# Kernel optimization log

Measured on AMD Instinct MI355X. Metric: run time of the kernel, lower is better.

Reference implementation:

```python
import jax, jax.numpy as jnp
import numpy as np

EPS = 1e-20


def setup_inputs() -> dict:
    B, N, V = 64, 8, 128000
    key = jax.random.key(0)
    k1, k2, k3 = jax.random.split(key, 3)
    draft_token_ids = jax.random.randint(k1, (B, N), 0, V, dtype=jnp.int64 if jax.config.jax_enable_x64 else jnp.int32)
    # proper probability distributions via softmax over random logits
    draft_probs = jax.nn.softmax(jax.random.normal(k2, (B, N, V), dtype=jnp.float32), axis=-1)
    verify_probs = jax.nn.softmax(jax.random.normal(k3, (B, N + 1, V), dtype=jnp.float32), axis=-1)
    return {
        "draft_token_ids": draft_token_ids,
        "draft_probs": draft_probs,
        "verify_probs": verify_probs,
    }


def reference(draft_token_ids, draft_probs, verify_probs):
    """Chain speculative (rejection) sampling, flashinfer-style.

    Returns:
      output_token_ids:  (B, N+1) int, rejected tail padded with -1
      accepted_token_num:(B,) independent per-token acceptance count
      emitted_token_num: (B,) accepted draft tokens before first rejection
    """
    B, N, V = draft_probs.shape
    key = jax.random.key(1)
    ku, kr, kb = jax.random.split(key, 3)

    tgt = verify_probs[:, :N, :]  # target probs aligned with draft positions
    # gather p = target prob of drafted token, q = draft prob of drafted token
    tok = draft_token_ids[..., None]
    p = jnp.take_along_axis(tgt, tok, axis=2)[..., 0]          # (B, N)
    q = jnp.take_along_axis(draft_probs, tok, axis=2)[..., 0]  # (B, N)

    u = jax.random.uniform(ku, (B, N), dtype=jnp.float32)
    accept = u * q < p                                          # (B, N) bool

    # independent-acceptance metric (alignment of draft vs target)
    accepted_token_num = accept.sum(axis=1).astype(jnp.int32)
    # chain: stop at first rejection
    prefix = jnp.cumprod(accept.astype(jnp.int32), axis=1)      # (B, N)
    emitted_token_num = prefix.sum(axis=1).astype(jnp.int32)    # (B,)

    # recovered distribution at each position: normalize relu(target - draft)
    residual = jnp.maximum(tgt - draft_probs, 0.0)
    residual = residual / jnp.maximum(residual.sum(axis=-1, keepdims=True), EPS)
    recovered = jax.random.categorical(kr, jnp.log(residual + EPS), axis=-1)  # (B, N)

    # bonus token from the extra target distribution (all drafts accepted)
    bonus = jax.random.categorical(kb, jnp.log(verify_probs[:, N, :] + EPS), axis=-1)  # (B,)

    batch_idx = jnp.arange(B)
    rec_at_stop = recovered[batch_idx, jnp.minimum(emitted_token_num, N - 1)]
    final_tok = jnp.where(emitted_token_num < N, rec_at_stop, bonus)  # (B,)

    pos = jnp.arange(N + 1)[None, :]                      # (1, N+1)
    em = emitted_token_num[:, None]                       # (B, 1)
    draft_ext = jnp.concatenate([draft_token_ids, jnp.zeros((B, 1), draft_token_ids.dtype)], axis=1)
    out = jnp.where(pos < em, draft_ext,
                    jnp.where(pos == em, final_tok[:, None].astype(draft_ext.dtype), -1))
    return out, accepted_token_num, emitted_token_num
```

## Files before the change

### kernel.cpp

```cpp
#include <hip/hip_runtime.h>
#include <stdint.h>

constexpr int Bn = 64;
constexpr int Nn = 8;
constexpr int Vn = 128000;
constexpr int CH = 32;
constexpr int CHUNK = Vn / CH;
constexpr int F4 = CHUNK / 4;
constexpr float EPSf = 1e-20f;
constexpr float TINYf = 1.17549435082228751e-38f;

struct TFOut { uint32_t a, b; };

__host__ __device__ constexpr TFOut tf2x32(uint32_t k0, uint32_t k1,
                                           uint32_t x0, uint32_t x1) {
  uint32_t k2 = k0 ^ k1 ^ 0x1BD11BDAu;
  x0 += k0; x1 += k1;
#define TFR(r) { x0 += x1; x1 = (uint32_t)((x1 << (r)) | (x1 >> (32 - (r)))); x1 ^= x0; }
  TFR(13) TFR(15) TFR(26) TFR(6)
  x0 += k1; x1 += k2 + 1u;
  TFR(17) TFR(29) TFR(16) TFR(24)
  x0 += k2; x1 += k0 + 2u;
  TFR(13) TFR(15) TFR(26) TFR(6)
  x0 += k0; x1 += k1 + 3u;
  TFR(17) TFR(29) TFR(16) TFR(24)
  x0 += k1; x1 += k2 + 4u;
  TFR(13) TFR(15) TFR(26) TFR(6)
  x0 += k2; x1 += k0 + 5u;
#undef TFR
  return TFOut{x0, x1};
}

constexpr TFOut KU = tf2x32(0u, 1u, 0u, 0u);
constexpr TFOut KR = tf2x32(0u, 1u, 0u, 1u);
constexpr TFOut KB_ = tf2x32(0u, 1u, 0u, 2u);

__device__ __forceinline__ float jax_u01(uint32_t bits) {
  return __uint_as_float((bits >> 9) | 0x3f800000u) - 1.0f;
}

__device__ __forceinline__ uint32_t rbits(uint32_t k0, uint32_t k1, uint32_t t) {
  TFOut o = tf2x32(k0, k1, 0u, t);
  return o.a ^ o.b;
}

__device__ __forceinline__ float gumbel_at(uint32_t k0, uint32_t k1, uint32_t t) {
  float u = jax_u01(rbits(k0, k1, t));
  float uu = fmaxf(TINYf, u + TINYf);
  return -logf(-logf(uu));
}

__device__ __forceinline__ unsigned long long packsc(float s, uint32_t v) {
  uint32_t u = __float_as_uint(s);
  uint32_t m = (u & 0x80000000u) ? ~u : (u | 0x80000000u);
  return ((unsigned long long)m << 32) | (unsigned long long)(~v);
}

__device__ __forceinline__ int accept_bit(int j, const int* __restrict__ ids,
                                          const float* __restrict__ draft,
                                          const float* __restrict__ verify) {
  int b = j >> 3, n = j & 7;
  float u = jax_u01(rbits(KU.a, KU.b, (uint32_t)j));
  int tok = ids[j];
  float p = verify[(size_t)(b * (Nn + 1) + n) * Vn + tok];
  float q = draft[(size_t)(b * Nn + n) * Vn + tok];
  return (u * q < p) ? 1 : 0;
}

__global__ void __launch_bounds__(256)
KA(const int* __restrict__ ids, const float* __restrict__ draft,
   const float* __restrict__ verify, int* __restrict__ out,
   float* __restrict__ partial, unsigned long long* __restrict__ R) {
  int blk = blockIdx.x;
  int b = blk >> 5, c = blk & 31;
  __shared__ int s_acc[8];
  __shared__ float sred[256];
  if (threadIdx.x < 8) s_acc[threadIdx.x] = accept_bit(b * 8 + threadIdx.x, ids, draft, verify);
  __syncthreads();
  int em = 0;
  while (em < 8 && s_acc[em]) em++;

  if (c == 0 && threadIdx.x == 0) {
    int acc = s_acc[0] + s_acc[1] + s_acc[2] + s_acc[3] + s_acc[4] + s_acc[5] + s_acc[6] + s_acc[7];
    out[Bn * (Nn + 1) + b] = acc;
    out[Bn * (Nn + 1) + Bn + b] = em;
    for (int pos = 0; pos <= Nn; pos++)
      out[b * (Nn + 1) + pos] = (pos < em) ? ids[b * Nn + pos] : -1;
    R[b] = 0ull;
  }
  if (em >= Nn) return;

  const float4* t4 = (const float4*)(verify + (size_t)(b * (Nn + 1) + em) * Vn + c * CHUNK);
  const float4* d4 = (const float4*)(draft + (size_t)(b * Nn + em) * Vn + c * CHUNK);
  float s = 0.0f;
  for (int i = threadIdx.x; i < F4; i += 256) {
    float4 t = t4[i], d = d4[i];
    s += fmaxf(t.x - d.x, 0.0f);
    s += fmaxf(t.y - d.y, 0.0f);
    s += fmaxf(t.z - d.z, 0.0f);
    s += fmaxf(t.w - d.w, 0.0f);
  }
  sred[threadIdx.x] = s;
  __syncthreads();
  for (int st = 128; st > 0; st >>= 1) {
    if (threadIdx.x < st) sred[threadIdx.x] += sred[threadIdx.x + st];
    __syncthreads();
  }
  if (threadIdx.x == 0) partial[blk] = sred[0];
}

__global__ void __launch_bounds__(256)
KB(const int* __restrict__ ids, const float* __restrict__ draft,
   const float* __restrict__ verify, const float* __restrict__ partial,
   unsigned long long* __restrict__ R) {
  int blk = blockIdx.x;
  int b = blk >> 5, c = blk & 31;
  __shared__ int s_acc[8];
  __shared__ unsigned long long smax[256];
  if (threadIdx.x < 8) s_acc[threadIdx.x] = accept_bit(b * 8 + threadIdx.x, ids, draft, verify);
  __syncthreads();
  int em = 0;
  while (em < 8 && s_acc[em]) em++;

  float best = -__builtin_inff();
  uint32_t bestv = 0u;

  if (em < Nn) {
    float S = 0.0f;
    for (int i = 0; i < CH; i++) S += partial[b * CH + i];
    float Sm = fmaxf(S, EPSf);
    const float4* t4 = (const float4*)(verify + (size_t)(b * (Nn + 1) + em) * Vn + c * CHUNK);
    const float4* d4 = (const float4*)(draft + (size_t)(b * Nn + em) * Vn + c * CHUNK);
    uint32_t trow = (uint32_t)(b * Nn + em) * (uint32_t)Vn;
    for (int i = threadIdx.x; i < F4; i += 256) {
      float4 t = t4[i], d = d4[i];
      uint32_t v0 = (uint32_t)(c * CHUNK + i * 4);
      float tv[4] = {t.x, t.y, t.z, t.w};
      float dv[4] = {d.x, d.y, d.z, d.w};
#pragma unroll
      for (int k = 0; k < 4; k++) {
        float r = fmaxf(tv[k] - dv[k], 0.0f);
        float logit = logf(r / Sm + EPSf);
        float sc = gumbel_at(KR.a, KR.b, trow + v0 + k) + logit;
        if (sc > best) { best = sc; bestv = v0 + k; }
      }
    }
  } else {
    const float4* p4 = (const float4*)(verify + (size_t)(b * (Nn + 1) + Nn) * Vn + c * CHUNK);
    uint32_t trow = (uint32_t)b * (uint32_t)Vn;
    for (int i = threadIdx.x; i < F4; i += 256) {
      float4 p = p4[i];
      uint32_t v0 = (uint32_t)(c * CHUNK + i * 4);
      float pv[4] = {p.x, p.y, p.z, p.w};
#pragma unroll
      for (int k = 0; k < 4; k++) {
        float logit = logf(pv[k] + EPSf);
        float sc = gumbel_at(KB_.a, KB_.b, trow + v0 + k) + logit;
        if (sc > best) { best = sc; bestv = v0 + k; }
      }
    }
  }

  smax[threadIdx.x] = packsc(best, bestv);
  __syncthreads();
  for (int st = 128; st > 0; st >>= 1) {
    if (threadIdx.x < st) {
      unsigned long long o = smax[threadIdx.x + st];
      if (o > smax[threadIdx.x]) smax[threadIdx.x] = o;
    }
    __syncthreads();
  }
  if (threadIdx.x == 0) atomicMax(&R[b], smax[0]);
}

__global__ void __launch_bounds__(512)
KC(const int* __restrict__ ids, const float* __restrict__ draft,
   const float* __restrict__ verify, const unsigned long long* __restrict__ R,
   int* __restrict__ out) {
  __shared__ int s_acc[512];
  int j = threadIdx.x;
  s_acc[j] = accept_bit(j, ids, draft, verify);
  __syncthreads();
  if (j < Bn) {
    int em = 0;
    while (em < 8 && s_acc[j * 8 + em]) em++;
    int tok = (int)(~(uint32_t)(R[j] & 0xFFFFFFFFull));
    out[j * (Nn + 1) + em] = tok;
  }
}

extern "C" void kernel_launch(void* const* d_in, const int* in_sizes, int n_in,
                              void* d_out, int out_size, void* d_ws, size_t ws_size,
                              hipStream_t stream) {
  const int* ids = (const int*)d_in[0];
  const float* draft = (const float*)d_in[1];
  const float* verify = (const float*)d_in[2];
  int* out = (int*)d_out;

  char* w = (char*)d_ws;
  float* partial = (float*)w;
  unsigned long long* R = (unsigned long long*)(w + 8192);

  KA<<<dim3(Bn * CH), dim3(256), 0, stream>>>(ids, draft, verify, out, partial, R);
  KB<<<dim3(Bn * CH), dim3(256), 0, stream>>>(ids, draft, verify, partial, R);
  KC<<<dim3(1), dim3(512), 0, stream>>>(ids, draft, verify, R, out);
}
```

Baseline: 472.7 us.

## Drop residual normalization and fuse sampling into one kernel with last-block finalize

Removes the separate residual-sum pass, since dividing by the sum is a constant shift of the logits and does not change the argmax. Rewrites the Gumbel-max score as log(x / -log u), which needs two logs per element instead of three. Merges the three kernels into one sampling kernel plus a tiny init kernel, using an atomic counter so the last block per row writes the final token. This cuts one full read of the two probability rows and a launch, at the risk of small float-rounding differences in the argmax when the EPS term interacts with normalization.

```diff
diff --git a/kernel.cpp b/kernel.cpp
--- a/kernel.cpp
+++ b/kernel.cpp
@@ -31,8 +31,8 @@
   return TFOut{x0, x1};
 }
 
-constexpr TFOut KU = tf2x32(0u, 1u, 0u, 0u);
-constexpr TFOut KR = tf2x32(0u, 1u, 0u, 1u);
+constexpr TFOut KU  = tf2x32(0u, 1u, 0u, 0u);
+constexpr TFOut KR  = tf2x32(0u, 1u, 0u, 1u);
 constexpr TFOut KB_ = tf2x32(0u, 1u, 0u, 2u);
 
 __device__ __forceinline__ float jax_u01(uint32_t bits) {
@@ -44,10 +44,10 @@
   return o.a ^ o.b;
 }
 
-__device__ __forceinline__ float gumbel_at(uint32_t k0, uint32_t k1, uint32_t t) {
+__device__ __forceinline__ float neglog_u(uint32_t k0, uint32_t k1, uint32_t t) {
   float u = jax_u01(rbits(k0, k1, t));
   float uu = fmaxf(TINYf, u + TINYf);
-  return -logf(-logf(uu));
+  return -logf(uu);
 }
 
 __device__ __forceinline__ unsigned long long packsc(float s, uint32_t v) {
@@ -67,14 +67,21 @@
   return (u * q < p) ? 1 : 0;
 }
 
+__global__ void __launch_bounds__(128)
+KInit(unsigned long long* __restrict__ R, unsigned int* __restrict__ cnt) {
+  int i = threadIdx.x;
+  if (i < Bn) R[i] = 0ull;
+  else if (i < 2 * Bn) cnt[i - Bn] = 0u;
+}
+
 __global__ void __launch_bounds__(256)
-KA(const int* __restrict__ ids, const float* __restrict__ draft,
+K1(const int* __restrict__ ids, const float* __restrict__ draft,
    const float* __restrict__ verify, int* __restrict__ out,
-   float* __restrict__ partial, unsigned long long* __restrict__ R) {
+   unsigned long long* __restrict__ R, unsigned int* __restrict__ cnt) {
   int blk = blockIdx.x;
   int b = blk >> 5, c = blk & 31;
   __shared__ int s_acc[8];
-  __shared__ float sred[256];
+  __shared__ unsigned long long smax[256];
   if (threadIdx.x < 8) s_acc[threadIdx.x] = accept_bit(b * 8 + threadIdx.x, ids, draft, verify);
   __syncthreads();
   int em = 0;
@@ -84,51 +91,14 @@
     int acc = s_acc[0] + s_acc[1] + s_acc[2] + s_acc[3] + s_acc[4] + s_acc[5] + s_acc[6] + s_acc[7];
     out[Bn * (Nn + 1) + b] = acc;
     out[Bn * (Nn + 1) + Bn + b] = em;
-    for (int pos = 0; pos <= Nn; pos++)
-      out[b * (Nn + 1) + pos] = (pos < em) ? ids[b * Nn + pos] : -1;
-    R[b] = 0ull;
+    for (int pos = 0; pos < em; pos++) out[b * (Nn + 1) + pos] = ids[b * Nn + pos];
+    for (int pos = em + 1; pos <= Nn; pos++) out[b * (Nn + 1) + pos] = -1;
   }
-  if (em >= Nn) return;
-
-  const float4* t4 = (const float4*)(verify + (size_t)(b * (Nn + 1) + em) * Vn + c * CHUNK);
-  const float4* d4 = (const float4*)(draft + (size_t)(b * Nn + em) * Vn + c * CHUNK);
-  float s = 0.0f;
-  for (int i = threadIdx.x; i < F4; i += 256) {
-    float4 t = t4[i], d = d4[i];
-    s += fmaxf(t.x - d.x, 0.0f);
-    s += fmaxf(t.y - d.y, 0.0f);
-    s += fmaxf(t.z - d.z, 0.0f);
-    s += fmaxf(t.w - d.w, 0.0f);
-  }
-  sred[threadIdx.x] = s;
-  __syncthreads();
-  for (int st = 128; st > 0; st >>= 1) {
-    if (threadIdx.x < st) sred[threadIdx.x] += sred[threadIdx.x + st];
-    __syncthreads();
-  }
-  if (threadIdx.x == 0) partial[blk] = sred[0];
-}
-
-__global__ void __launch_bounds__(256)
-KB(const int* __restrict__ ids, const float* __restrict__ draft,
-   const float* __restrict__ verify, const float* __restrict__ partial,
-   unsigned long long* __restrict__ R) {
-  int blk = blockIdx.x;
-  int b = blk >> 5, c = blk & 31;
-  __shared__ int s_acc[8];
-  __shared__ unsigned long long smax[256];
-  if (threadIdx.x < 8) s_acc[threadIdx.x] = accept_bit(b * 8 + threadIdx.x, ids, draft, verify);
-  __syncthreads();
-  int em = 0;
-  while (em < 8 && s_acc[em]) em++;
 
   float best = -__builtin_inff();
   uint32_t bestv = 0u;
 
   if (em < Nn) {
-    float S = 0.0f;
-    for (int i = 0; i < CH; i++) S += partial[b * CH + i];
-    float Sm = fmaxf(S, EPSf);
     const float4* t4 = (const float4*)(verify + (size_t)(b * (Nn + 1) + em) * Vn + c * CHUNK);
     const float4* d4 = (const float4*)(draft + (size_t)(b * Nn + em) * Vn + c * CHUNK);
     uint32_t trow = (uint32_t)(b * Nn + em) * (uint32_t)Vn;
@@ -139,9 +109,9 @@
       float dv[4] = {d.x, d.y, d.z, d.w};
 #pragma unroll
       for (int k = 0; k < 4; k++) {
-        float r = fmaxf(tv[k] - dv[k], 0.0f);
-        float logit = logf(r / Sm + EPSf);
-        float sc = gumbel_at(KR.a, KR.b, trow + v0 + k) + logit;
+        float x = fmaxf(tv[k] - dv[k], 0.0f) + EPSf;
+        float nl = neglog_u(KR.a, KR.b, trow + v0 + k);
+        float sc = logf(x / nl);
         if (sc > best) { best = sc; bestv = v0 + k; }
       }
     }
@@ -154,8 +124,9 @@
       float pv[4] = {p.x, p.y, p.z, p.w};
 #pragma unroll
       for (int k = 0; k < 4; k++) {
-        float logit = logf(pv[k] + EPSf);
-        float sc = gumbel_at(KB_.a, KB_.b, trow + v0 + k) + logit;
+        float x = pv[k] + EPSf;
+        float nl = neglog_u(KB_.a, KB_.b, trow + v0 + k);
+        float sc = logf(x / nl);
         if (sc > best) { best = sc; bestv = v0 + k; }
       }
     }
@@ -170,22 +141,14 @@
     }
     __syncthreads();
   }
-  if (threadIdx.x == 0) atomicMax(&R[b], smax[0]);
-}
 
-__global__ void __launch_bounds__(512)
-KC(const int* __restrict__ ids, const float* __restrict__ draft,
-   const float* __restrict__ verify, const unsigned long long* __restrict__ R,
-   int* __restrict__ out) {
-  __shared__ int s_acc[512];
-  int j = threadIdx.x;
-  s_acc[j] = accept_bit(j, ids, draft, verify);
-  __syncthreads();
-  if (j < Bn) {
-    int em = 0;
-    while (em < 8 && s_acc[j * 8 + em]) em++;
-    int tok = (int)(~(uint32_t)(R[j] & 0xFFFFFFFFull));
-    out[j * (Nn + 1) + em] = tok;
+  if (threadIdx.x == 0) {
+    atomicMax(&R[b], smax[0]);
+    __threadfence();
+    if (atomicAdd(&cnt[b], 1u) == (unsigned)(CH - 1)) {
+      unsigned long long v = atomicMax(&R[b], 0ull);
+      out[b * (Nn + 1) + em] = (int)(~(uint32_t)(v & 0xFFFFFFFFull));
+    }
   }
 }
 
@@ -198,10 +161,9 @@
   int* out = (int*)d_out;
 
   char* w = (char*)d_ws;
-  float* partial = (float*)w;
-  unsigned long long* R = (unsigned long long*)(w + 8192);
+  unsigned long long* R = (unsigned long long*)w;
+  unsigned int* cnt = (unsigned int*)(w + Bn * 8);
 
-  KA<<<dim3(Bn * CH), dim3(256), 0, stream>>>(ids, draft, verify, out, partial, R);
-  KB<<<dim3(Bn * CH), dim3(256), 0, stream>>>(ids, draft, verify, partial, R);
-  KC<<<dim3(1), dim3(512), 0, stream>>>(ids, draft, verify, R, out);
+  KInit<<<dim3(1), dim3(128), 0, stream>>>(R, cnt);
+  K1<<<dim3(Bn * CH), dim3(256), 0, stream>>>(ids, draft, verify, out, R, cnt);
 }
```

After: 511.2 us. +8.1%, slower.
